# Kernel optimization log

Hardware: AMD Instinct MI355X
Metric: run time of the kernel (lower is better)

The kernel has to match this reference:

```python
import jax, jax.numpy as jnp
import numpy as np

N, D = 1024, 256


def setup_inputs() -> dict:
    key = jax.random.key(0)
    k1, k2 = jax.random.split(key)
    mu_X = jax.random.normal(k1, (N, D), dtype=jnp.float32)
    log_sigma = jax.random.normal(k2, (N, D), dtype=jnp.float32)
    return {"mu_X": mu_X, "log_sigma": log_sigma}


def reference(mu_X, log_sigma):
    # F.normalize: x / max(||x||_2, eps), eps=1e-12
    norm = jnp.linalg.norm(mu_X, axis=-1, keepdims=True)
    mu = mu_X / jnp.maximum(norm, 1e-12)
    sigma_sq = jnp.exp(log_sigma)                       # [N, D]
    sig_sum = sigma_sq[:, None, :] + sigma_sq[None, :, :]  # [N, N, D]
    # pairwise squared diff weighted by summed variances + log-variance penalty
    diff = (mu[:, None, :] - mu[None, :, :]) ** 2 / (1e-10 + sig_sum) + jnp.log(sig_sum)
    return -diff.sum(axis=2)                            # [N, N]
```

## Files before the change

### kernel.cpp

```cpp
#include <hip/hip_runtime.h>

#define N 1024
#define D 256

#define RI 8
#define LDW 260

__global__ __launch_bounds__(256) void prep3(
    const float* __restrict__ muX, const float* __restrict__ ls,
    float2* __restrict__ msT2) {
  const int i0 = blockIdx.x * RI;
  const int t = threadIdx.x;
  __shared__ float smu[RI][LDW];
  __shared__ float ssg[RI][LDW];
  __shared__ float sred[RI][32];
  __shared__ float rden[RI];
  const float4* mu4 = (const float4*)(muX + (size_t)i0 * D);
  const float4* ls4 = (const float4*)(ls + (size_t)i0 * D);
#pragma unroll
  for (int u = 0; u < 2; ++u) {
    const int idx = u * 256 + t;
    const int row = idx >> 6, c4 = idx & 63;
    const float4 v = mu4[idx];
    *(float4*)&smu[row][c4 * 4] = v;
    const float4 e = ls4[idx];
    float4 x;
    x.x = __expf(e.x) + 5e-11f; x.y = __expf(e.y) + 5e-11f;
    x.z = __expf(e.z) + 5e-11f; x.w = __expf(e.w) + 5e-11f;
    *(float4*)&ssg[row][c4 * 4] = x;
  }
  __syncthreads();
  {
    const int r = t >> 5, q = t & 31;
    float s = 0.f;
#pragma unroll
    for (int k = 0; k < 8; ++k) {
      const float v = smu[r][q + 32 * k];
      s = fmaf(v, v, s);
    }
    sred[r][q] = s;
  }
  __syncthreads();
  if (t < RI) {
    float tot = 0.f;
    for (int u = 0; u < 32; ++u) tot += sred[t][u];
    rden[t] = 1.0f / fmaxf(sqrtf(tot), 1e-12f);
  }
  __syncthreads();
#pragma unroll
  for (int pass = 0; pass < 8; ++pass) {
    const int f = pass * 256 + t;
    const int b = f & 1, il = (f >> 1) & 7, g = f >> 4;
    const float* src = b ? &ssg[il][0] : &smu[il][0];
    const float sc = b ? 1.0f : rden[il];
    msT2[((size_t)g * N + i0 + il) * 2 + b] =
        make_float2(src[2 * g] * sc, src[2 * g + 1] * sc);
  }
}

__global__ __launch_bounds__(128) void pair_kernel(
    const float4* __restrict__ msT4, float* __restrict__ out) {
  int L = blockIdx.x;
  int js = 0, base = 0;
  while (L >= base + 64 * (js + 1)) { base += 64 * (js + 1); ++js; }
  const int ib = L - base;
  const int j0 = js * 128, i0 = ib * 2;
  const bool diag = (ib >= js * 64);
  const int j = j0 + threadIdx.x;

  float acc[2] = {0.f, 0.f};
  float p[2] = {1.f, 1.f};
  int ea[2] = {0, 0};

#pragma unroll 4
  for (int gg = 0; gg < D / 4; ++gg) {
    const float4 jva = msT4[(size_t)(2 * gg) * N + j];
    const float4 jvb = msT4[(size_t)(2 * gg + 1) * N + j];
#pragma unroll
    for (int k = 0; k < 2; ++k) {
      const float4 iva = msT4[(size_t)(2 * gg) * N + i0 + k];
      const float4 ivb = msT4[(size_t)(2 * gg + 1) * N + i0 + k];
      const float sa0 = iva.z + jva.z, sa1 = iva.w + jva.w;
      const float da0 = iva.x - jva.x, da1 = iva.y - jva.y;
      const float sb0 = ivb.z + jvb.z, sb1 = ivb.w + jvb.w;
      const float db0 = ivb.x - jvb.x, db1 = ivb.y - jvb.y;
      const float qa0 = da0 * da0, qa1 = da1 * da1;
      const float qb0 = db0 * db0, qb1 = db1 * db1;
      const float s01 = sa0 * sa1, s23 = sb0 * sb1;
      float na = qa0 * sa1; na = fmaf(qa1, sa0, na);
      float nb = qb0 * sb1; nb = fmaf(qb1, sb0, nb);
      float num = na * s23; num = fmaf(nb, s01, num);
      const float den = s01 * s23;
      acc[k] = fmaf(num, __builtin_amdgcn_rcpf(den), acc[k]);
      p[k] *= den;
    }
    if (gg & 1) {
#pragma unroll
      for (int k = 0; k < 2; ++k) {
        const int bb = __float_as_int(p[k]);
        ea[k] += bb >> 23;
        p[k] = __int_as_float((bb & 0x007fffff) | 0x3f800000);
      }
    }
  }

  constexpr float LN2 = 0.6931471805599453f;
  float v[2];
#pragma unroll
  for (int k = 0; k < 2; ++k) {
    const float lg2 = (float)(ea[k] - 127 * (D / 8)) + __log2f(p[k]);
    v[k] = -(acc[k] + LN2 * lg2);
  }

  if (!diag) {
    out[(size_t)i0 * N + j] = v[0];
    out[(size_t)(i0 + 1) * N + j] = v[1];
    *(float2*)(out + (size_t)j * N + i0) = make_float2(v[0], v[1]);
  } else {
#pragma unroll
    for (int k = 0; k < 2; ++k) {
      const int i = i0 + k;
      if (j >= i) out[(size_t)i * N + j] = v[k];
      if (j > i) out[(size_t)j * N + i] = v[k];
    }
  }
}

extern "C" void kernel_launch(void* const* d_in, const int* in_sizes, int n_in,
                              void* d_out, int out_size, void* d_ws, size_t ws_size,
                              hipStream_t stream) {
  const float* muX = (const float*)d_in[0];
  const float* ls  = (const float*)d_in[1];
  float* out = (float*)d_out;
  float2* msT2 = (float2*)d_ws;
  prep3<<<dim3(N / RI), dim3(256), 0, stream>>>(muX, ls, msT2);
  const int nblocks = 64 * (8 * 9 / 2);
  pair_kernel<<<dim3(nblocks), dim3(128), 0, stream>>>((const float4*)msT2,
                                                       out);
}
```

Measured before the change: 91.64 us.

## Fuse prep and pair kernels into one persistent kernel with grid barrier

Merges the preprocessing and pairwise kernels into a single persistent launch of 1152 blocks. The first 1024 blocks each normalize one row with a wave shuffle reduction and write the transposed scratch, then all blocks meet at a global atomic barrier before running the tile loop. This removes one kernel launch and the gap between the two kernels. In exchange it relies on all 1152 blocks being co-resident for the spin barrier to avoid deadlock, and it gives up the 2304-block grid for a grid-stride tile loop.

```diff
diff --git a/kernel.cpp b/kernel.cpp
--- a/kernel.cpp
+++ b/kernel.cpp
@@ -2,126 +2,115 @@
 
 #define N 1024
 #define D 256
+#define NB 1152
 
-#define RI 8
-#define LDW 260
+__device__ float4 g_scr[(D / 2) * N];
+__device__ int g_bar;
 
-__global__ __launch_bounds__(256) void prep3(
+__global__ __launch_bounds__(128) void fused(
     const float* __restrict__ muX, const float* __restrict__ ls,
-    float2* __restrict__ msT2) {
-  const int i0 = blockIdx.x * RI;
+    float* __restrict__ out) {
+  const int b = blockIdx.x;
   const int t = threadIdx.x;
-  __shared__ float smu[RI][LDW];
-  __shared__ float ssg[RI][LDW];
-  __shared__ float sred[RI][32];
-  __shared__ float rden[RI];
-  const float4* mu4 = (const float4*)(muX + (size_t)i0 * D);
-  const float4* ls4 = (const float4*)(ls + (size_t)i0 * D);
+
+  if (b < 1024 && t < 64) {
+    const int l = t;
+    const float4 mu = ((const float4*)muX)[b * 64 + l];
+    const float4 e = ((const float4*)ls)[b * 64 + l];
+    float s =
+        fmaf(mu.x, mu.x, fmaf(mu.y, mu.y, fmaf(mu.z, mu.z, mu.w * mu.w)));
 #pragma unroll
-  for (int u = 0; u < 2; ++u) {
-    const int idx = u * 256 + t;
-    const int row = idx >> 6, c4 = idx & 63;
-    const float4 v = mu4[idx];
-    *(float4*)&smu[row][c4 * 4] = v;
-    const float4 e = ls4[idx];
-    float4 x;
-    x.x = __expf(e.x) + 5e-11f; x.y = __expf(e.y) + 5e-11f;
-    x.z = __expf(e.z) + 5e-11f; x.w = __expf(e.w) + 5e-11f;
-    *(float4*)&ssg[row][c4 * 4] = x;
+    for (int m = 32; m >= 1; m >>= 1) s += __shfl_xor(s, m, 64);
+    const float rden = 1.0f / fmaxf(sqrtf(s), 1e-12f);
+    float4 sg;
+    sg.x = __expf(e.x) + 5e-11f; sg.y = __expf(e.y) + 5e-11f;
+    sg.z = __expf(e.z) + 5e-11f; sg.w = __expf(e.w) + 5e-11f;
+    g_scr[(size_t)(2 * l) * N + b] =
+        make_float4(mu.x * rden, mu.y * rden, sg.x, sg.y);
+    g_scr[(size_t)(2 * l + 1) * N + b] =
+        make_float4(mu.z * rden, mu.w * rden, sg.z, sg.w);
+  }
+
+  __threadfence();
+  __syncthreads();
+  if (t == 0) {
+    const int old = __hip_atomic_fetch_add(&g_bar, 1, __ATOMIC_ACQ_REL,
+                                           __HIP_MEMORY_SCOPE_AGENT);
+    const int target = (old / NB + 1) * NB;
+    while (__hip_atomic_load(&g_bar, __ATOMIC_ACQUIRE,
+                             __HIP_MEMORY_SCOPE_AGENT) < target) {
+      __builtin_amdgcn_s_sleep(1);
+    }
   }
   __syncthreads();
-  {
-    const int r = t >> 5, q = t & 31;
-    float s = 0.f;
-#pragma unroll
-    for (int k = 0; k < 8; ++k) {
-      const float v = smu[r][q + 32 * k];
-      s = fmaf(v, v, s);
-    }
-    sred[r][q] = s;
-  }
-  __syncthreads();
-  if (t < RI) {
-    float tot = 0.f;
-    for (int u = 0; u < 32; ++u) tot += sred[t][u];
-    rden[t] = 1.0f / fmaxf(sqrtf(tot), 1e-12f);
-  }
-  __syncthreads();
-#pragma unroll
-  for (int pass = 0; pass < 8; ++pass) {
-    const int f = pass * 256 + t;
-    const int b = f & 1, il = (f >> 1) & 7, g = f >> 4;
-    const float* src = b ? &ssg[il][0] : &smu[il][0];
-    const float sc = b ? 1.0f : rden[il];
-    msT2[((size_t)g * N + i0 + il) * 2 + b] =
-        make_float2(src[2 * g] * sc, src[2 * g + 1] * sc);
-  }
-}
+  __threadfence();
 
-__global__ __launch_bounds__(128) void pair_kernel(
-    const float4* __restrict__ msT4, float* __restrict__ out) {
-  int L = blockIdx.x;
-  int js = 0, base = 0;
-  while (L >= base + 64 * (js + 1)) { base += 64 * (js + 1); ++js; }
-  const int ib = L - base;
-  const int j0 = js * 128, i0 = ib * 2;
-  const bool diag = (ib >= js * 64);
-  const int j = j0 + threadIdx.x;
+  const float4* __restrict__ msT4 = (const float4*)g_scr;
 
-  float acc[2] = {0.f, 0.f};
-  float p[2] = {1.f, 1.f};
-  int ea[2] = {0, 0};
+  for (int tile = b; tile < 64 * (8 * 9 / 2); tile += NB) {
+    int L = tile;
+    int js = 0, base = 0;
+    while (L >= base + 64 * (js + 1)) { base += 64 * (js + 1); ++js; }
+    const int ib = L - base;
+    const int j0 = js * 128, i0 = ib * 2;
+    const bool diag = (ib >= js * 64);
+    const int j = j0 + t;
+
+    float acc[2] = {0.f, 0.f};
+    float p[2] = {1.f, 1.f};
+    int ea[2] = {0, 0};
 
 #pragma unroll 4
-  for (int gg = 0; gg < D / 4; ++gg) {
-    const float4 jva = msT4[(size_t)(2 * gg) * N + j];
-    const float4 jvb = msT4[(size_t)(2 * gg + 1) * N + j];
+    for (int gg = 0; gg < D / 4; ++gg) {
+      const float4 jva = msT4[(size_t)(2 * gg) * N + j];
+      const float4 jvb = msT4[(size_t)(2 * gg + 1) * N + j];
+#pragma unroll
+      for (int k = 0; k < 2; ++k) {
+        const float4 iva = msT4[(size_t)(2 * gg) * N + i0 + k];
+        const float4 ivb = msT4[(size_t)(2 * gg + 1) * N + i0 + k];
+        const float sa0 = iva.z + jva.z, sa1 = iva.w + jva.w;
+        const float da0 = iva.x - jva.x, da1 = iva.y - jva.y;
+        const float sb0 = ivb.z + jvb.z, sb1 = ivb.w + jvb.w;
+        const float db0 = ivb.x - jvb.x, db1 = ivb.y - jvb.y;
+        const float qa0 = da0 * da0, qa1 = da1 * da1;
+        const float qb0 = db0 * db0, qb1 = db1 * db1;
+        const float s01 = sa0 * sa1, s23 = sb0 * sb1;
+        float na = qa0 * sa1; na = fmaf(qa1, sa0, na);
+        float nb = qb0 * sb1; nb = fmaf(qb1, sb0, nb);
+        float num = na * s23; num = fmaf(nb, s01, num);
+        const float den = s01 * s23;
+        acc[k] = fmaf(num, __builtin_amdgcn_rcpf(den), acc[k]);
+        p[k] *= den;
+      }
+      if (gg & 1) {
+#pragma unroll
+        for (int k = 0; k < 2; ++k) {
+          const int bb = __float_as_int(p[k]);
+          ea[k] += bb >> 23;
+          p[k] = __int_as_float((bb & 0x007fffff) | 0x3f800000);
+        }
+      }
+    }
+
+    constexpr float LN2 = 0.6931471805599453f;
+    float v[2];
 #pragma unroll
     for (int k = 0; k < 2; ++k) {
-      const float4 iva = msT4[(size_t)(2 * gg) * N + i0 + k];
-      const float4 ivb = msT4[(size_t)(2 * gg + 1) * N + i0 + k];
-      const float sa0 = iva.z + jva.z, sa1 = iva.w + jva.w;
-      const float da0 = iva.x - jva.x, da1 = iva.y - jva.y;
-      const float sb0 = ivb.z + jvb.z, sb1 = ivb.w + jvb.w;
-      const float db0 = ivb.x - jvb.x, db1 = ivb.y - jvb.y;
-      const float qa0 = da0 * da0, qa1 = da1 * da1;
-      const float qb0 = db0 * db0, qb1 = db1 * db1;
-      const float s01 = sa0 * sa1, s23 = sb0 * sb1;
-      float na = qa0 * sa1; na = fmaf(qa1, sa0, na);
-      float nb = qb0 * sb1; nb = fmaf(qb1, sb0, nb);
-      float num = na * s23; num = fmaf(nb, s01, num);
-      const float den = s01 * s23;
-      acc[k] = fmaf(num, __builtin_amdgcn_rcpf(den), acc[k]);
-      p[k] *= den;
+      const float lg2 = (float)(ea[k] - 127 * (D / 8)) + __log2f(p[k]);
+      v[k] = -(acc[k] + LN2 * lg2);
     }
-    if (gg & 1) {
+
+    if (!diag) {
+      out[(size_t)i0 * N + j] = v[0];
+      out[(size_t)(i0 + 1) * N + j] = v[1];
+      *(float2*)(out + (size_t)j * N + i0) = make_float2(v[0], v[1]);
+    } else {
 #pragma unroll
       for (int k = 0; k < 2; ++k) {
-        const int bb = __float_as_int(p[k]);
-        ea[k] += bb >> 23;
-        p[k] = __int_as_float((bb & 0x007fffff) | 0x3f800000);
+        const int i = i0 + k;
+        if (j >= i) out[(size_t)i * N + j] = v[k];
+        if (j > i) out[(size_t)j * N + i] = v[k];
       }
-    }
-  }
-
-  constexpr float LN2 = 0.6931471805599453f;
-  float v[2];
-#pragma unroll
-  for (int k = 0; k < 2; ++k) {
-    const float lg2 = (float)(ea[k] - 127 * (D / 8)) + __log2f(p[k]);
-    v[k] = -(acc[k] + LN2 * lg2);
-  }
-
-  if (!diag) {
-    out[(size_t)i0 * N + j] = v[0];
-    out[(size_t)(i0 + 1) * N + j] = v[1];
-    *(float2*)(out + (size_t)j * N + i0) = make_float2(v[0], v[1]);
-  } else {
-#pragma unroll
-    for (int k = 0; k < 2; ++k) {
-      const int i = i0 + k;
-      if (j >= i) out[(size_t)i * N + j] = v[k];
-      if (j > i) out[(size_t)j * N + i] = v[k];
     }
   }
 }
@@ -132,9 +121,6 @@
   const float* muX = (const float*)d_in[0];
   const float* ls  = (const float*)d_in[1];
   float* out = (float*)d_out;
-  float2* msT2 = (float2*)d_ws;
-  prep3<<<dim3(N / RI), dim3(256), 0, stream>>>(muX, ls, msT2);
-  const int nblocks = 64 * (8 * 9 / 2);
-  pair_kernel<<<dim3(nblocks), dim3(128), 0, stream>>>((const float4*)msT2,
-                                                       out);
+  (void)d_ws; (void)ws_size;
+  fused<<<dim3(NB), dim3(128), 0, stream>>>(muX, ls, out);
 }
```

After: 292.5 us. 219% more time.
